# Performance work log

Measured on AMD Instinct MI355X. Metric: run time of the kernel, lower is better.

The kernel has to match this reference:

```python
import jax, jax.numpy as jnp
import numpy as np

N_NODES = 50000
N_EDGES = 800000
IN_CH = 128
OUT_CH = 64
HEADS = 4
NEG_SLOPE = 0.2  # PyG GATConv default


def setup_inputs() -> dict:
    key = jax.random.key(0)
    k1, k2, k3, k4, k5 = jax.random.split(key, 5)
    x = jax.random.normal(k1, (N_NODES, IN_CH), dtype=jnp.float32)
    edge_index = jax.random.randint(k2, (2, N_EDGES), 0, N_NODES, dtype=jnp.int64)
    W = jax.random.normal(k3, (HEADS * OUT_CH, IN_CH), dtype=jnp.float32) * (1.0 / np.sqrt(IN_CH))
    att_src = jax.random.normal(k4, (HEADS, OUT_CH), dtype=jnp.float32) * (1.0 / np.sqrt(OUT_CH))
    att_dst = jax.random.normal(k5, (HEADS, OUT_CH), dtype=jnp.float32) * (1.0 / np.sqrt(OUT_CH))
    bias = jnp.zeros((OUT_CH,), dtype=jnp.float32)
    return {"x": x, "edge_index": edge_index, "W": W,
            "att_src": att_src, "att_dst": att_dst, "bias": bias}


def reference(x, edge_index, W, att_src, att_dst, bias):
    # GAT2NO_NORM.forward in eval mode: dropout == identity.
    N = x.shape[0]
    H, C = att_src.shape
    # PyG GATConv adds self-loops by default.
    loop = jnp.arange(N, dtype=edge_index.dtype)
    src = jnp.concatenate([edge_index[0], loop])  # message source j
    dst = jnp.concatenate([edge_index[1], loop])  # message target i
    # Linear projection, reshape to heads: [N, H, C]
    h = (x @ W.T).reshape(N, H, C)
    # Per-node attention halves: [N, H]
    a_src = jnp.einsum('nhc,hc->nh', h, att_src)
    a_dst = jnp.einsum('nhc,hc->nh', h, att_dst)
    # Per-edge raw score, LeakyReLU: [E, H]
    e = jax.nn.leaky_relu(a_src[src] + a_dst[dst], NEG_SLOPE)
    # Segment (edge-)softmax over incoming edges of each dst node.
    m = jax.lax.stop_gradient(jax.ops.segment_max(e, dst, num_segments=N))
    ex = jnp.exp(e - m[dst])
    denom = jax.ops.segment_sum(ex, dst, num_segments=N)
    alpha = ex / denom[dst]  # self-loops guarantee denom > 0
    # Weighted scatter-sum of messages: [N, H, C]
    msg = h[src] * alpha[:, :, None]
    out = jax.ops.segment_sum(msg, dst, num_segments=N)
    # concat=False -> mean over heads, then bias, then ReLU (module wrapper)
    out = out.mean(axis=1) + bias
    return jax.nn.relu(out)
```

## Files before the change

kernel.cpp:

```cpp
#include <hip/hip_runtime.h>
#include <hip/hip_fp16.h>
#include <math.h>

#define N_NODES 50000
#define N_EDGES 800000
#define IN_CH 128
#define PROJ_CH 256
#define OUT_CH 64
#define HEADS 4
#define NEG_SLOPE 0.2f
#define CAP 80
#define PROJ_BLOCKS 782
#define EPB 1024

typedef _Float16 f16x8 __attribute__((ext_vector_type(8)));
typedef _Float16 f16x4 __attribute__((ext_vector_type(4)));
typedef float    f32x4 __attribute__((ext_vector_type(4)));

__device__ __forceinline__ float leaky(float v) {
    return v > 0.f ? v : NEG_SLOPE * v;
}

__global__ __launch_bounds__(256) void prep_kernel(
    const float* __restrict__ W, _Float16* __restrict__ Wfrag, int* __restrict__ cnt)
{
    int t = blockIdx.x * 256 + threadIdx.x;
    if (t < N_NODES) cnt[t] = 0;
    if (t < 4096) {
        int lane = t & 63;
        int n0i  = (t >> 6) & 3;
        int w    = (t >> 8) & 3;
        int k0i  = t >> 10;
        int oc = w * 64 + n0i * 16 + (lane & 15);
        int kb = k0i * 32 + (lane >> 4) * 8;
        const float* src = W + (size_t)oc * IN_CH + kb;
        f16x8 v;
#pragma unroll
        for (int j = 0; j < 8; ++j) v[j] = (_Float16)src[j];
        *(f16x8*)(Wfrag + (size_t)t * 8) = v;
    }
}

__global__ __launch_bounds__(256) void proj_fill_kernel(
    const float* __restrict__ x, const _Float16* __restrict__ Wfrag,
    const float* __restrict__ att_src, const float* __restrict__ att_dst,
    const int* __restrict__ ei, int* __restrict__ cnt, unsigned short* __restrict__ csr,
    _Float16* __restrict__ h, float* __restrict__ a_src, float* __restrict__ a_dst)
{
    __shared__ _Float16 xs[64 * 136];
    const int tid  = threadIdx.x;
    const int w    = tid >> 6;
    const int lane = tid & 63;
    const int q    = lane >> 4;
    const int l15  = lane & 15;
    const int nb   = blockIdx.x * 64;

    int esrc[4], edst[4];
    const int ebase = blockIdx.x * EPB + tid;
#pragma unroll
    for (int k = 0; k < 4; ++k) {
        int e = ebase + k * 256;
        if (e < N_EDGES) { esrc[k] = ei[e]; edst[k] = ei[N_EDGES + e]; }
        else edst[k] = -1;
    }

    f16x8 B[4][4];
#pragma unroll
    for (int k0i = 0; k0i < 4; ++k0i)
#pragma unroll
        for (int n0i = 0; n0i < 4; ++n0i)
            B[k0i][n0i] = *(const f16x8*)(Wfrag +
                (size_t)(((k0i * 4 + w) * 4 + n0i) * 64 + lane) * 8);

#pragma unroll
    for (int r = 0; r < 8; ++r) {
        int v   = r * 256 + tid;
        int row = v >> 5;
        int c4  = v & 31;
        int grow = nb + row;
        if (grow > N_NODES - 1) grow = N_NODES - 1;
        float4 xv = *(const float4*)(x + (size_t)grow * IN_CH + c4 * 4);
        f16x4 hv;
        hv[0] = (_Float16)xv.x; hv[1] = (_Float16)xv.y;
        hv[2] = (_Float16)xv.z; hv[3] = (_Float16)xv.w;
        *(f16x4*)&xs[row * 136 + c4 * 4] = hv;
    }
    __syncthreads();

    f32x4 acc[4][4];
#pragma unroll
    for (int m0i = 0; m0i < 4; ++m0i)
#pragma unroll
        for (int n0i = 0; n0i < 4; ++n0i)
            acc[m0i][n0i] = (f32x4){0.f, 0.f, 0.f, 0.f};

#pragma unroll
    for (int k0i = 0; k0i < 4; ++k0i) {
        f16x8 A[4];
#pragma unroll
        for (int m0i = 0; m0i < 4; ++m0i)
            A[m0i] = *(const f16x8*)&xs[(m0i * 16 + l15) * 136 + k0i * 32 + q * 8];
#pragma unroll
        for (int n0i = 0; n0i < 4; ++n0i)
#pragma unroll
            for (int m0i = 0; m0i < 4; ++m0i)
                acc[m0i][n0i] = __builtin_amdgcn_mfma_f32_16x16x32_f16(
                    A[m0i], B[k0i][n0i], acc[m0i][n0i], 0, 0, 0);
    }

    float att_s[4], att_d[4];
#pragma unroll
    for (int n0i = 0; n0i < 4; ++n0i) {
        att_s[n0i] = att_src[w * 64 + n0i * 16 + l15];
        att_d[n0i] = att_dst[w * 64 + n0i * 16 + l15];
    }

#pragma unroll
    for (int m0i = 0; m0i < 4; ++m0i) {
        float vs[4], vd[4];
#pragma unroll
        for (int r = 0; r < 4; ++r) {
            float s = 0.f, d = 0.f;
#pragma unroll
            for (int n0i = 0; n0i < 4; ++n0i) {
                s = fmaf(acc[m0i][n0i][r], att_s[n0i], s);
                d = fmaf(acc[m0i][n0i][r], att_d[n0i], d);
            }
            vs[r] = s; vd[r] = d;
        }
#pragma unroll
        for (int off = 1; off < 16; off <<= 1) {
#pragma unroll
            for (int r = 0; r < 4; ++r) {
                vs[r] += __shfl_xor(vs[r], off, 64);
                vd[r] += __shfl_xor(vd[r], off, 64);
            }
        }
#pragma unroll
        for (int r = 0; r < 4; ++r) {
            int node = nb + m0i * 16 + q * 4 + r;
            if (l15 == 0 && node < N_NODES) {
                a_src[node * HEADS + w] = vs[r];
                a_dst[node * HEADS + w] = vd[r];
            }
        }
#pragma unroll
        for (int r = 0; r < 4; ++r) {
            int node = nb + m0i * 16 + q * 4 + r;
            if (node < N_NODES) {
#pragma unroll
                for (int n0i = 0; n0i < 4; ++n0i)
                    h[(size_t)node * PROJ_CH + w * 64 + n0i * 16 + l15] =
                        (_Float16)acc[m0i][n0i][r];
            }
        }
    }

#pragma unroll
    for (int k = 0; k < 4; ++k) {
        if (edst[k] >= 0) {
            int pos = atomicAdd(&cnt[edst[k]], 1);
            if (pos < CAP) csr[edst[k] * CAP + pos] = (unsigned short)esrc[k];
        }
    }
}

__global__ __launch_bounds__(256) void aggregate_kernel(
    const _Float16* __restrict__ h, const float* __restrict__ a_src,
    const float* __restrict__ a_dst, const int* __restrict__ cnt,
    const unsigned short* __restrict__ csr, const float* __restrict__ bias,
    float* __restrict__ out)
{
    const int tid  = threadIdx.x;
    const int wave = tid >> 6;
    const int l    = tid & 63;
    const int i    = blockIdx.x * 4 + wave;

    __shared__ float lw_all[4][(CAP + 1) * 4];
    __shared__ int   lj_all[4][CAP + 1 + 3];
    float* lw = lw_all[wave];
    int*   lj = lj_all[wave];

    const int n    = min(cnt[i], CAP);
    const int base = i * CAP;
    const int h4   = l & 3;
    const float adh = a_dst[i * 4 + h4];

    float lsum = 0.f;
    {
        float ws = __expf(leaky(a_src[i * 4 + h4] + adh));
        if (l < 4) { lw[l] = ws; lsum = ws; }
        if (l == 0) lj[0] = i;
    }

    const int erel = l >> 2;
    for (int p0 = 0; p0 < n; p0 += 16) {
        int e = p0 + erel;
        bool valid = e < n;
        int j = valid ? (int)csr[base + e] : 0;
        float w = 0.f;
        if (valid) w = __expf(leaky(a_src[j * 4 + h4] + adh));
        lsum += w;
        lw[(e + 1) * 4 + h4] = w;
        if (h4 == 0) lj[e + 1] = j;
    }
#pragma unroll
    for (int off = 4; off < 64; off <<= 1) lsum += __shfl_xor(lsum, off, 64);

    __syncthreads();

    const int half_ = l >> 5;
    const int jj    = l & 31;
    const int hd    = jj >> 3;
    const int m_total = n + 1;
    const uint4* hv = (const uint4*)h;

    float acc[8];
#pragma unroll
    for (int k = 0; k < 8; ++k) acc[k] = 0.f;

    for (int qq = 0; qq < m_total; qq += 4) {
        int e0 = qq + half_;
        int e1 = e0 + 2;
        int i0 = (e0 < m_total) ? e0 : 0;
        int i1 = (e1 < m_total) ? e1 : 0;
        float w0 = (e0 < m_total) ? lw[i0 * 4 + hd] : 0.f;
        float w1 = (e1 < m_total) ? lw[i1 * 4 + hd] : 0.f;
        int j0 = lj[i0];
        int j1 = lj[i1];
        uint4 d0 = hv[(size_t)j0 * 32 + jj];
        uint4 d1 = hv[(size_t)j1 * 32 + jj];
        float2 a0 = __half22float2(*(const __half2*)&d0.x);
        float2 a1 = __half22float2(*(const __half2*)&d0.y);
        float2 a2 = __half22float2(*(const __half2*)&d0.z);
        float2 a3 = __half22float2(*(const __half2*)&d0.w);
        acc[0] = fmaf(w0, a0.x, acc[0]);
        acc[1] = fmaf(w0, a0.y, acc[1]);
        acc[2] = fmaf(w0, a1.x, acc[2]);
        acc[3] = fmaf(w0, a1.y, acc[3]);
        acc[4] = fmaf(w0, a2.x, acc[4]);
        acc[5] = fmaf(w0, a2.y, acc[5]);
        acc[6] = fmaf(w0, a3.x, acc[6]);
        acc[7] = fmaf(w0, a3.y, acc[7]);
        float2 b0 = __half22float2(*(const __half2*)&d1.x);
        float2 b1 = __half22float2(*(const __half2*)&d1.y);
        float2 b2 = __half22float2(*(const __half2*)&d1.z);
        float2 b3 = __half22float2(*(const __half2*)&d1.w);
        acc[0] = fmaf(w1, b0.x, acc[0]);
        acc[1] = fmaf(w1, b0.y, acc[1]);
        acc[2] = fmaf(w1, b1.x, acc[2]);
        acc[3] = fmaf(w1, b1.y, acc[3]);
        acc[4] = fmaf(w1, b2.x, acc[4]);
        acc[5] = fmaf(w1, b2.y, acc[5]);
        acc[6] = fmaf(w1, b3.x, acc[6]);
        acc[7] = fmaf(w1, b3.y, acc[7]);
    }

#pragma unroll
    for (int k = 0; k < 8; ++k) acc[k] += __shfl_xor(acc[k], 32, 64);

    float linv = 1.f / __shfl(lsum, hd, 64);
#pragma unroll
    for (int k = 0; k < 8; ++k) {
        float r = acc[k] * linv;
        r += __shfl_xor(r, 8, 64);
        r += __shfl_xor(r, 16, 64);
        acc[k] = r;
    }

    if (l < 8) {
        float* op = out + (size_t)i * OUT_CH + l * 8;
        float4 o0, o1;
        o0.x = fmaxf(0.25f * acc[0] + bias[l * 8 + 0], 0.f);
        o0.y = fmaxf(0.25f * acc[1] + bias[l * 8 + 1], 0.f);
        o0.z = fmaxf(0.25f * acc[2] + bias[l * 8 + 2], 0.f);
        o0.w = fmaxf(0.25f * acc[3] + bias[l * 8 + 3], 0.f);
        o1.x = fmaxf(0.25f * acc[4] + bias[l * 8 + 4], 0.f);
        o1.y = fmaxf(0.25f * acc[5] + bias[l * 8 + 5], 0.f);
        o1.z = fmaxf(0.25f * acc[6] + bias[l * 8 + 6], 0.f);
        o1.w = fmaxf(0.25f * acc[7] + bias[l * 8 + 7], 0.f);
        *(float4*)op = o0;
        *((float4*)op + 1) = o1;
    }
}

extern "C" void kernel_launch(void* const* d_in, const int* in_sizes, int n_in,
                              void* d_out, int out_size, void* d_ws, size_t ws_size,
                              hipStream_t stream)
{
    const float* x       = (const float*)d_in[0];
    const int*   ei      = (const int*)d_in[1];
    const float* W       = (const float*)d_in[2];
    const float* att_src = (const float*)d_in[3];
    const float* att_dst = (const float*)d_in[4];
    const float* bias    = (const float*)d_in[5];
    float* out = (float*)d_out;

    _Float16* h     = (_Float16*)d_ws;
    _Float16* Wfrag = h + (size_t)N_NODES * PROJ_CH;
    float* asrc  = (float*)(Wfrag + 4096 * 8);
    float* adst  = asrc + (size_t)N_NODES * HEADS;
    int*   cnt   = (int*)(adst + (size_t)N_NODES * HEADS);
    unsigned short* csr = (unsigned short*)(cnt + N_NODES);

    hipLaunchKernelGGL(prep_kernel, dim3(196), dim3(256), 0, stream,
                       W, Wfrag, cnt);
    hipLaunchKernelGGL(proj_fill_kernel, dim3(PROJ_BLOCKS), dim3(256), 0, stream,
                       x, Wfrag, att_src, att_dst, ei, cnt, csr, h, asrc, adst);
    hipLaunchKernelGGL(aggregate_kernel, dim3(N_NODES / 4), dim3(256), 0, stream,
                       h, asrc, adst, cnt, csr, bias, out);
}
```

Measured before the change: 206.3 us.

## Split edge CSR fill across extra blocks and overlap atomic with MFMA

The fused projection+CSR-fill kernel now launches 3125 blocks, one edge per thread. The first 782 blocks still do the projection, and the remaining blocks only do the atomic count and CSR write. In projection blocks the atomicAdd is issued before the MFMA loop so its latency overlaps the matrix work, with the CSR store after. This spreads the atomic-heavy scatter over many more waves, at the cost of the projection blocks holding an extra live register through the GEMM.

```diff
diff --git a/kernel.cpp b/kernel.cpp
--- a/kernel.cpp
+++ b/kernel.cpp
@@ -11,7 +11,7 @@
 #define NEG_SLOPE 0.2f
 #define CAP 80
 #define PROJ_BLOCKS 782
-#define EPB 1024
+#define GRID_BLOCKS 3125
 
 typedef _Float16 f16x8 __attribute__((ext_vector_type(8)));
 typedef _Float16 f16x4 __attribute__((ext_vector_type(4)));
@@ -41,28 +41,31 @@
     }
 }
 
-__global__ __launch_bounds__(256) void proj_fill_kernel(
+__global__ __launch_bounds__(256) void mega_kernel(
     const float* __restrict__ x, const _Float16* __restrict__ Wfrag,
     const float* __restrict__ att_src, const float* __restrict__ att_dst,
     const int* __restrict__ ei, int* __restrict__ cnt, unsigned short* __restrict__ csr,
     _Float16* __restrict__ h, float* __restrict__ a_src, float* __restrict__ a_dst)
 {
     __shared__ _Float16 xs[64 * 136];
-    const int tid  = threadIdx.x;
+    const int tid = threadIdx.x;
+    const int bid = blockIdx.x;
+
+    const int e = bid * 256 + tid;
+    const int esrc = ei[e];
+    const int edst = ei[N_EDGES + e];
+
+    if (bid >= PROJ_BLOCKS) {
+        int pos = atomicAdd(&cnt[edst], 1);
+        if (pos < CAP) csr[edst * CAP + pos] = (unsigned short)esrc;
+        return;
+    }
+
     const int w    = tid >> 6;
     const int lane = tid & 63;
     const int q    = lane >> 4;
     const int l15  = lane & 15;
-    const int nb   = blockIdx.x * 64;
-
-    int esrc[4], edst[4];
-    const int ebase = blockIdx.x * EPB + tid;
-#pragma unroll
-    for (int k = 0; k < 4; ++k) {
-        int e = ebase + k * 256;
-        if (e < N_EDGES) { esrc[k] = ei[e]; edst[k] = ei[N_EDGES + e]; }
-        else edst[k] = -1;
-    }
+    const int nb   = bid * 64;
 
     f16x8 B[4][4];
 #pragma unroll
@@ -87,6 +90,8 @@
     }
     __syncthreads();
 
+    const int pos = atomicAdd(&cnt[edst], 1);
+
     f32x4 acc[4][4];
 #pragma unroll
     for (int m0i = 0; m0i < 4; ++m0i)
@@ -156,13 +161,7 @@
         }
     }
 
-#pragma unroll
-    for (int k = 0; k < 4; ++k) {
-        if (edst[k] >= 0) {
-            int pos = atomicAdd(&cnt[edst[k]], 1);
-            if (pos < CAP) csr[edst[k] * CAP + pos] = (unsigned short)esrc[k];
-        }
-    }
+    if (pos < CAP) csr[edst * CAP + pos] = (unsigned short)esrc;
 }
 
 __global__ __launch_bounds__(256) void aggregate_kernel(
@@ -305,7 +304,7 @@
 
     hipLaunchKernelGGL(prep_kernel, dim3(196), dim3(256), 0, stream,
                        W, Wfrag, cnt);
-    hipLaunchKernelGGL(proj_fill_kernel, dim3(PROJ_BLOCKS), dim3(256), 0, stream,
+    hipLaunchKernelGGL(mega_kernel, dim3(GRID_BLOCKS), dim3(256), 0, stream,
                        x, Wfrag, att_src, att_dst, ei, cnt, csr, h, asrc, adst);
     hipLaunchKernelGGL(aggregate_kernel, dim3(N_NODES / 4), dim3(256), 0, stream,
                        h, asrc, adst, cnt, csr, bias, out);
```

Measured after the change: 206.4 us. Within noise of the previous version (+0.0%).
